# Performance work log

Hardware: AMD Instinct MI355X
Metric: run time of the kernel (lower is better)

Reference implementation:

```python
import jax, jax.numpy as jnp
import numpy as np


def setup_inputs() -> dict:
    key = jax.random.key(0)
    k1, k2, k3, k4, k5 = jax.random.split(key, 5)
    B, N, M, D = 16, 8192, 8192, 256
    emb = jax.random.normal(k1, (B, M, D), dtype=jnp.float32)
    pts = jax.random.normal(k2, (B, N, 5), dtype=jnp.float32)
    num = jax.random.randint(k3, (B,), 1, M + 1)
    indeces = jax.random.randint(k4, (B, M), 0, N)
    W = jax.random.normal(k5, (4, D), dtype=jnp.float32) * (1.414 / np.sqrt(4 + D))
    image_shape = jnp.array([B, 3, 768, 1024], dtype=jnp.int64)  # (b, c, H, W)
    return {"emb": emb, "num": num, "pts": pts, "indeces": indeces,
            "image_shape": image_shape, "W": W}


def reference(emb, num, pts, indeces, image_shape, W):
    height = image_shape[2].astype(jnp.float32)
    width = image_shape[3].astype(jnp.float32)
    # normalize_keypoints: center at image center, scale by 0.7*max(W,H)
    size = jnp.stack([width, height])                      # [2] (w, h)
    center = size / 2.0
    scaling = jnp.max(size) * 0.7
    upts = (pts[..., :2] - center) / scaling               # [B,N,2]
    # normalize_angle: (angle - 45) / (180*0.7)
    uangle = (pts[..., 4:5] - 45.0) / (180.0 * 0.7)        # [B,N,1]
    # normalize_len: scale by 0.7*diag, center at half that
    diag = jnp.sqrt(width * width + height * height)
    lscale = diag * 0.7
    ulen = (pts[..., 3:4] - lscale / 2.0) / lscale         # [B,N,1]
    feat = jnp.concatenate([upts, uangle, ulen], axis=-1)  # [B,N,4]
    pose_feature = jnp.einsum("bnf,fd->bnd", feat, W)      # [B,N,D]
    # per-batch gather of pose_feature rows, added to first num[b] emb slots
    gathered = jnp.take_along_axis(pose_feature, indeces[..., None], axis=1)  # [B,M,D]
    slot = jnp.arange(emb.shape[1])[None, :]               # [1,M]
    mask = (slot < num[:, None])[..., None]                # [B,M,1]
    return emb + jnp.where(mask, gathered, 0.0)
```

## Files before the change

kernel.cpp:

```cpp
#include <hip/hip_runtime.h>


#define DD 256

__global__ __launch_bounds__(256) void posfeat_d256_kernel(
    const float* __restrict__ emb,
    const int* __restrict__ num,
    const float* __restrict__ pts,
    const int* __restrict__ indeces,
    const int* __restrict__ image_shape,
    const float* __restrict__ W,
    float* __restrict__ out,
    int B, int M, int N)
{
    const int lane = threadIdx.x & 63;
    const int wave = threadIdx.x >> 6;
    const int b = blockIdx.y;
    const int base_m = (blockIdx.x * 4 + wave) * 8;
    if (base_m >= M) return;

    const float h = (float)image_shape[2];
    const float w = (float)image_shape[3];
    const float inv_s  = 1.0f / (fmaxf(w, h) * 0.7f);
    const float cx = w * 0.5f, cy = h * 0.5f;
    const float lscale = sqrtf(w * w + h * h) * 0.7f;
    const float inv_l  = 1.0f / lscale;
    const float half_l = lscale * 0.5f;
    const float inv_a  = 1.0f / 126.0f;

    const int d0 = lane * 4;
    const float4 w0 = *(const float4*)(W + 0 * DD + d0);
    const float4 w1 = *(const float4*)(W + 1 * DD + d0);
    const float4 w2 = *(const float4*)(W + 2 * DD + d0);
    const float4 w3 = *(const float4*)(W + 3 * DD + d0);

    const int nb = num[b];

    int idxv = -1;
    if (lane < 8) {
        const int m = base_m + lane;
        if (m < M && m < nb) idxv = indeces[(long long)b * M + m];
    }
    float pv = 0.f;
    {
        const int r = lane / 5, c = lane - r * 5;
        const int ir = __shfl(idxv, r);
        if (lane < 40 && ir >= 0)
            pv = pts[((long long)b * N + ir) * 5 + c];
    }

    const long long baseoff = ((long long)b * M + base_m) * DD + d0;
    const int nrows = (M - base_m < 8) ? (M - base_m) : 8;

    float4 e[8];
    #pragma unroll
    for (int r = 0; r < 8; ++r)
        if (r < nrows) e[r] = *(const float4*)(emb + baseoff + (long long)r * DD);

    #pragma unroll
    for (int r = 0; r < 8; ++r) {
        if (r >= nrows) continue;
        const int   ir = __shfl(idxv, r);
        const float p0 = __shfl(pv, r * 5 + 0);
        const float p1 = __shfl(pv, r * 5 + 1);
        const float p3 = __shfl(pv, r * 5 + 3);
        const float p4 = __shfl(pv, r * 5 + 4);
        float f0 = 0.f, f1 = 0.f, f2 = 0.f, f3 = 0.f;
        if (ir >= 0) {
            f0 = (p0 - cx) * inv_s;
            f1 = (p1 - cy) * inv_s;
            f2 = (p4 - 45.0f) * inv_a;
            f3 = (p3 - half_l) * inv_l;
        }
        float4 o;
        o.x = e[r].x + f0 * w0.x + f1 * w1.x + f2 * w2.x + f3 * w3.x;
        o.y = e[r].y + f0 * w0.y + f1 * w1.y + f2 * w2.y + f3 * w3.y;
        o.z = e[r].z + f0 * w0.z + f1 * w1.z + f2 * w2.z + f3 * w3.z;
        o.w = e[r].w + f0 * w0.w + f1 * w1.w + f2 * w2.w + f3 * w3.w;
        *(float4*)(out + baseoff + (long long)r * DD) = o;
    }
}

__global__ __launch_bounds__(256) void posfeat_generic_kernel(
    const float* __restrict__ emb, const int* __restrict__ num,
    const float* __restrict__ pts, const int* __restrict__ indeces,
    const int* __restrict__ image_shape, const float* __restrict__ W,
    float* __restrict__ out, int B, int M, int N, int D)
{
    const int lane = threadIdx.x & 63;
    const int wave = threadIdx.x >> 6;
    const int m = blockIdx.x * 4 + wave;
    const int b = blockIdx.y;
    if (m >= M) return;
    const float h = (float)image_shape[2];
    const float w = (float)image_shape[3];
    const float inv_s = 1.0f / (fmaxf(w, h) * 0.7f);
    const float cx = w * 0.5f, cy = h * 0.5f;
    const float lscale = sqrtf(w * w + h * h) * 0.7f;
    const float inv_l = 1.0f / lscale;
    const float inv_a = 1.0f / 126.0f;
    float f0 = 0.f, f1 = 0.f, f2 = 0.f, f3 = 0.f;
    if (m < num[b]) {
        const int idx = indeces[(long long)b * M + m];
        const float* p = pts + ((long long)b * N + (long long)idx) * 5;
        f0 = (p[0] - cx) * inv_s;
        f1 = (p[1] - cy) * inv_s;
        f2 = (p[4] - 45.0f) * inv_a;
        f3 = (p[3] - lscale * 0.5f) * inv_l;
    }
    const long long rowoff = ((long long)b * M + m) * (long long)D;
    for (int dd = lane * 4; dd < D; dd += 64 * 4) {
        const float4 w0 = *(const float4*)(W + 0 * D + dd);
        const float4 w1 = *(const float4*)(W + 1 * D + dd);
        const float4 w2 = *(const float4*)(W + 2 * D + dd);
        const float4 w3 = *(const float4*)(W + 3 * D + dd);
        const float4 e  = *(const float4*)(emb + rowoff + dd);
        float4 r;
        r.x = e.x + f0 * w0.x + f1 * w1.x + f2 * w2.x + f3 * w3.x;
        r.y = e.y + f0 * w0.y + f1 * w1.y + f2 * w2.y + f3 * w3.y;
        r.z = e.z + f0 * w0.z + f1 * w1.z + f2 * w2.z + f3 * w3.z;
        r.w = e.w + f0 * w0.w + f1 * w1.w + f2 * w2.w + f3 * w3.w;
        *(float4*)(out + rowoff + dd) = r;
    }
}

extern "C" void kernel_launch(void* const* d_in, const int* in_sizes, int n_in,
                              void* d_out, int out_size, void* d_ws, size_t ws_size,
                              hipStream_t stream) {
    (void)n_in; (void)d_ws; (void)ws_size; (void)out_size;
    const float* emb  = (const float*)d_in[0];
    const int*   num  = (const int*)d_in[1];
    const float* pts  = (const float*)d_in[2];
    const int*   idx  = (const int*)d_in[3];
    const int*   ishp = (const int*)d_in[4];
    const float* Wm   = (const float*)d_in[5];
    float*       out  = (float*)d_out;

    const int B = in_sizes[1];
    const int D = in_sizes[5] / 4;
    const int M = (int)((long long)in_sizes[3] / B);
    const int N = (int)((long long)in_sizes[2] / ((long long)B * 5));

    if (D == 256) {
        dim3 block(256);
        dim3 grid((M + 31) / 32, B);
        hipLaunchKernelGGL(posfeat_d256_kernel, grid, block, 0, stream,
                           emb, num, pts, idx, ishp, Wm, out, B, M, N);
    } else {
        dim3 block(256);
        dim3 grid((M + 3) / 4, B);
        hipLaunchKernelGGL(posfeat_generic_kernel, grid, block, 0, stream,
                           emb, num, pts, idx, ishp, Wm, out, B, M, N, D);
    }
}
```

Baseline: 48.12 us.

## Use persistent grid-stride tiles and nontemporal stores in D=256 kernel

Replaces the 2D grid of one-tile-per-wave blocks with a 1D persistent grid capped at 2048 blocks, where each wave loops over flattened (batch, 8-row) tiles. Output writes become nontemporal stores through a clang vector type, so the streamed output is meant to bypass cache retention. The aim is to cut block launch overhead and cache pollution in a purely bandwidth-bound kernel. The cost is that each wave now handles several tiles in sequence, which can reduce the number of loads in flight per wave.

```diff
diff --git a/kernel.cpp b/kernel.cpp
--- a/kernel.cpp
+++ b/kernel.cpp
@@ -1,5 +1,7 @@
 #include <hip/hip_runtime.h>
 
+
+typedef float f32x4 __attribute__((ext_vector_type(4)));
 
 #define DD 256
 
@@ -11,13 +13,11 @@
     const int* __restrict__ image_shape,
     const float* __restrict__ W,
     float* __restrict__ out,
-    int B, int M, int N)
+    int B, int M, int N, int tiles_per_b, int total_tiles)
 {
     const int lane = threadIdx.x & 63;
     const int wave = threadIdx.x >> 6;
-    const int b = blockIdx.y;
-    const int base_m = (blockIdx.x * 4 + wave) * 8;
-    if (base_m >= M) return;
+    const int waves_per_grid = gridDim.x * 4;
 
     const float h = (float)image_shape[2];
     const float w = (float)image_shape[3];
@@ -29,55 +29,58 @@
     const float inv_a  = 1.0f / 126.0f;
 
     const int d0 = lane * 4;
-    const float4 w0 = *(const float4*)(W + 0 * DD + d0);
-    const float4 w1 = *(const float4*)(W + 1 * DD + d0);
-    const float4 w2 = *(const float4*)(W + 2 * DD + d0);
-    const float4 w3 = *(const float4*)(W + 3 * DD + d0);
+    const f32x4 w0 = *(const f32x4*)(W + 0 * DD + d0);
+    const f32x4 w1 = *(const f32x4*)(W + 1 * DD + d0);
+    const f32x4 w2 = *(const f32x4*)(W + 2 * DD + d0);
+    const f32x4 w3 = *(const f32x4*)(W + 3 * DD + d0);
 
-    const int nb = num[b];
+    const int pr = lane / 5, pc = lane - pr * 5;
 
-    int idxv = -1;
-    if (lane < 8) {
-        const int m = base_m + lane;
-        if (m < M && m < nb) idxv = indeces[(long long)b * M + m];
-    }
-    float pv = 0.f;
-    {
-        const int r = lane / 5, c = lane - r * 5;
-        const int ir = __shfl(idxv, r);
-        if (lane < 40 && ir >= 0)
-            pv = pts[((long long)b * N + ir) * 5 + c];
-    }
+    for (int tile = blockIdx.x * 4 + wave; tile < total_tiles; tile += waves_per_grid) {
+        const int b      = tile / tiles_per_b;
+        const int base_m = (tile - b * tiles_per_b) * 8;
+        const int nb     = num[b];
 
-    const long long baseoff = ((long long)b * M + base_m) * DD + d0;
-    const int nrows = (M - base_m < 8) ? (M - base_m) : 8;
+        int idxv = -1;
+        if (lane < 8) {
+            const int m = base_m + lane;
+            if (m < M && m < nb) idxv = indeces[(long long)b * M + m];
+        }
+        const int ir_g = __shfl(idxv, pr);
+        float pv = 0.f;
+        if (lane < 40 && ir_g >= 0)
+            pv = pts[((long long)b * N + ir_g) * 5 + pc];
 
-    float4 e[8];
-    #pragma unroll
-    for (int r = 0; r < 8; ++r)
-        if (r < nrows) e[r] = *(const float4*)(emb + baseoff + (long long)r * DD);
+        const long long baseoff = ((long long)b * M + base_m) * DD + d0;
+        const int nrows = (M - base_m < 8) ? (M - base_m) : 8;
 
-    #pragma unroll
-    for (int r = 0; r < 8; ++r) {
-        if (r >= nrows) continue;
-        const int   ir = __shfl(idxv, r);
-        const float p0 = __shfl(pv, r * 5 + 0);
-        const float p1 = __shfl(pv, r * 5 + 1);
-        const float p3 = __shfl(pv, r * 5 + 3);
-        const float p4 = __shfl(pv, r * 5 + 4);
-        float f0 = 0.f, f1 = 0.f, f2 = 0.f, f3 = 0.f;
-        if (ir >= 0) {
-            f0 = (p0 - cx) * inv_s;
-            f1 = (p1 - cy) * inv_s;
-            f2 = (p4 - 45.0f) * inv_a;
-            f3 = (p3 - half_l) * inv_l;
+        f32x4 e[8];
+        #pragma unroll
+        for (int r = 0; r < 8; ++r)
+            if (r < nrows) e[r] = *(const f32x4*)(emb + baseoff + (long long)r * DD);
+
+        #pragma unroll
+        for (int r = 0; r < 8; ++r) {
+            if (r >= nrows) continue;
+            const int   ir = __shfl(idxv, r);
+            const float p0 = __shfl(pv, r * 5 + 0);
+            const float p1 = __shfl(pv, r * 5 + 1);
+            const float p3 = __shfl(pv, r * 5 + 3);
+            const float p4 = __shfl(pv, r * 5 + 4);
+            float f0 = 0.f, f1 = 0.f, f2 = 0.f, f3 = 0.f;
+            if (ir >= 0) {
+                f0 = (p0 - cx) * inv_s;
+                f1 = (p1 - cy) * inv_s;
+                f2 = (p4 - 45.0f) * inv_a;
+                f3 = (p3 - half_l) * inv_l;
+            }
+            f32x4 o;
+            o.x = e[r].x + f0 * w0.x + f1 * w1.x + f2 * w2.x + f3 * w3.x;
+            o.y = e[r].y + f0 * w0.y + f1 * w1.y + f2 * w2.y + f3 * w3.y;
+            o.z = e[r].z + f0 * w0.z + f1 * w1.z + f2 * w2.z + f3 * w3.z;
+            o.w = e[r].w + f0 * w0.w + f1 * w1.w + f2 * w2.w + f3 * w3.w;
+            __builtin_nontemporal_store(o, (f32x4*)(out + baseoff + (long long)r * DD));
         }
-        float4 o;
-        o.x = e[r].x + f0 * w0.x + f1 * w1.x + f2 * w2.x + f3 * w3.x;
-        o.y = e[r].y + f0 * w0.y + f1 * w1.y + f2 * w2.y + f3 * w3.y;
-        o.z = e[r].z + f0 * w0.z + f1 * w1.z + f2 * w2.z + f3 * w3.z;
-        o.w = e[r].w + f0 * w0.w + f1 * w1.w + f2 * w2.w + f3 * w3.w;
-        *(float4*)(out + baseoff + (long long)r * DD) = o;
     }
 }
 
@@ -110,17 +113,17 @@
     }
     const long long rowoff = ((long long)b * M + m) * (long long)D;
     for (int dd = lane * 4; dd < D; dd += 64 * 4) {
-        const float4 w0 = *(const float4*)(W + 0 * D + dd);
-        const float4 w1 = *(const float4*)(W + 1 * D + dd);
-        const float4 w2 = *(const float4*)(W + 2 * D + dd);
-        const float4 w3 = *(const float4*)(W + 3 * D + dd);
-        const float4 e  = *(const float4*)(emb + rowoff + dd);
-        float4 r;
+        const f32x4 w0 = *(const f32x4*)(W + 0 * D + dd);
+        const f32x4 w1 = *(const f32x4*)(W + 1 * D + dd);
+        const f32x4 w2 = *(const f32x4*)(W + 2 * D + dd);
+        const f32x4 w3 = *(const f32x4*)(W + 3 * D + dd);
+        const f32x4 e  = *(const f32x4*)(emb + rowoff + dd);
+        f32x4 r;
         r.x = e.x + f0 * w0.x + f1 * w1.x + f2 * w2.x + f3 * w3.x;
         r.y = e.y + f0 * w0.y + f1 * w1.y + f2 * w2.y + f3 * w3.y;
         r.z = e.z + f0 * w0.z + f1 * w1.z + f2 * w2.z + f3 * w3.z;
         r.w = e.w + f0 * w0.w + f1 * w1.w + f2 * w2.w + f3 * w3.w;
-        *(float4*)(out + rowoff + dd) = r;
+        *(f32x4*)(out + rowoff + dd) = r;
     }
 }
 
@@ -142,10 +145,13 @@
     const int N = (int)((long long)in_sizes[2] / ((long long)B * 5));
 
     if (D == 256) {
-        dim3 block(256);
-        dim3 grid((M + 31) / 32, B);
-        hipLaunchKernelGGL(posfeat_d256_kernel, grid, block, 0, stream,
-                           emb, num, pts, idx, ishp, Wm, out, B, M, N);
+        const int tiles_per_b = (M + 7) / 8;
+        const int total_tiles = B * tiles_per_b;
+        int blocks = (total_tiles + 3) / 4;
+        if (blocks > 2048) blocks = 2048;
+        hipLaunchKernelGGL(posfeat_d256_kernel, dim3(blocks), dim3(256), 0, stream,
+                           emb, num, pts, idx, ishp, Wm, out, B, M, N,
+                           tiles_per_b, total_tiles);
     } else {
         dim3 block(256);
         dim3 grid((M + 3) / 4, B);
```

Result: faster. 46.79 us (-2.8%).
